# Kernel tuning notes

Hardware: AMD Instinct MI355X
Metric: run time of the kernel (lower is better)

The kernel has to match this reference:

```python
import jax, jax.numpy as jnp
import numpy as np

N_NODES = 50000


def gcn_conv(x, W, b, src, dst, n_nodes):
    # PyG GCNConv: y = D^-1/2 (A + I) D^-1/2 (x @ W) + b, with D counting self-loops
    h = x @ W                                             # [N, out]
    deg = jnp.ones((n_nodes,), h.dtype).at[dst].add(1.0)  # in-degree + self-loop
    dinv = jax.lax.rsqrt(deg)
    norm = dinv[src] * dinv[dst]                          # [E]
    msg = h[src] * norm[:, None]                          # [E, out]
    out = jnp.zeros_like(h).at[dst].add(msg)              # scatter-add over edges
    out = out + h * (dinv * dinv)[:, None]                # self-loop contribution
    return out + b


def setup_inputs() -> dict:
    key = jax.random.key(0)
    k = jax.random.split(key, 7)
    d_in, d_hid, d_out = 128, 128, 64
    x = jax.random.normal(k[0], (N_NODES, d_in), jnp.float32)
    edge_index = jax.random.randint(k[1], (2, 800000), 0, N_NODES, jnp.int64)
    s1 = 1.0 / np.sqrt(d_in)
    s2 = 1.0 / np.sqrt(d_hid)
    W1 = jax.random.uniform(k[2], (d_in, d_hid), jnp.float32, -s1, s1)
    b1 = jnp.zeros((d_hid,), jnp.float32)
    W2 = jax.random.uniform(k[3], (d_hid, d_out), jnp.float32, -s2, s2)
    b2 = jnp.zeros((d_out,), jnp.float32)
    return {"x": x, "edge_index": edge_index, "W1": W1, "b1": b1, "W2": W2, "b2": b2}


def reference(x, edge_index, W1, b1, W2, b2):
    src, dst = edge_index[0], edge_index[1]
    h = jax.nn.relu(gcn_conv(x, W1, b1, src, dst, N_NODES))
    h = gcn_conv(h, W2, b2, src, dst, N_NODES)
    return jax.nn.log_softmax(h, axis=1)
```

## Files before the change

### kernel.cpp

```cpp
#include <hip/hip_runtime.h>
#include <hip/hip_bf16.h>
#include <math.h>


typedef unsigned int uint32;
typedef unsigned short ushort16;
typedef unsigned char uchar;
typedef __attribute__((ext_vector_type(8))) short bf16x8;
typedef __attribute__((ext_vector_type(4))) float f32x4;

__device__ inline unsigned short f2bf_rne(float f) {
    uint32 x = __float_as_uint(f);
    uint32 r = (x + 0x7fffu + ((x >> 16) & 1u)) >> 16;
    return (unsigned short)r;
}
__device__ inline uint32 pack_bf16x2(float a, float b) {
    return (uint32)f2bf_rne(a) | ((uint32)f2bf_rne(b) << 16);
}
__device__ inline float2 unpack_bf16x2(uint32 u) {
    float2 r;
    r.x = __uint_as_float(u << 16);
    r.y = __uint_as_float(u & 0xffff0000u);
    return r;
}

#define NHB 128

__global__ __launch_bounds__(256) void hist_conv_k(const int* __restrict__ dst, int E,
                                                   int NWb, int chunk,
                                                   uint32* __restrict__ counts_pb,
                                                   uchar* __restrict__ rankx,
                                                   const float* __restrict__ W1,
                                                   const float* __restrict__ W2,
                                                   unsigned short* __restrict__ W1t,
                                                   unsigned short* __restrict__ W2t) {
    const int tid = threadIdx.x;
    if ((int)blockIdx.x >= 4 * NHB) {
        int idx = ((int)blockIdx.x - 4 * NHB) * 256 + tid;
        if (idx < 128 * 128) {
            int ns = idx >> 7, k = idx & 127;
            int t = ns >> 4, m = ns & 15;
            int col = 32 * (t >> 1) + 2 * m + (t & 1);
            W1t[idx] = f2bf_rne(W1[k * 128 + col]);
        } else {
            int i2 = idx - 128 * 128;
            if (i2 < 64 * 128) {
                int ns = i2 >> 7, k = i2 & 127;
                int t = ns >> 4, m = ns & 15;
                int col = 32 * (t >> 1) + 2 * m + (t & 1);
                W2t[i2] = f2bf_rne(W2[k * 64 + col]);
            }
        }
        return;
    }
    extern __shared__ uint32 sh[];
    const int hb  = blockIdx.x >> 2;
    const int qt  = blockIdx.x & 3;
    const int NWq = (NWb + 3) >> 2;
    const int qlo = qt * NWq;
    const int qhi = min(NWb, qlo + NWq);
    const int qn  = qhi - qlo;
    for (int i = tid; i < qn; i += 256) sh[i] = 0;
    __syncthreads();
    const int e0 = hb * chunk;
    const int e1 = min(E, e0 + chunk);
    int e = e0 + tid;
    for (; e + 768 < e1; e += 1024) {
        int d0 = dst[e];
        int d1 = dst[e + 256];
        int d2 = dst[e + 512];
        int d3 = dst[e + 768];
        int w0 = d0 >> 2, w1 = d1 >> 2, w2 = d2 >> 2, w3 = d3 >> 2;
        if (w0 >= qlo && w0 < qhi) {
            uint32 o = atomicAdd(&sh[w0 - qlo], 1u << (8 * (d0 & 3)));
            rankx[e] = (uchar)(o >> (8 * (d0 & 3)));
        }
        if (w1 >= qlo && w1 < qhi) {
            uint32 o = atomicAdd(&sh[w1 - qlo], 1u << (8 * (d1 & 3)));
            rankx[e + 256] = (uchar)(o >> (8 * (d1 & 3)));
        }
        if (w2 >= qlo && w2 < qhi) {
            uint32 o = atomicAdd(&sh[w2 - qlo], 1u << (8 * (d2 & 3)));
            rankx[e + 512] = (uchar)(o >> (8 * (d2 & 3)));
        }
        if (w3 >= qlo && w3 < qhi) {
            uint32 o = atomicAdd(&sh[w3 - qlo], 1u << (8 * (d3 & 3)));
            rankx[e + 768] = (uchar)(o >> (8 * (d3 & 3)));
        }
    }
    for (; e < e1; e += 256) {
        int d = dst[e];
        int w = d >> 2;
        if (w >= qlo && w < qhi) {
            uint32 o = atomicAdd(&sh[w - qlo], 1u << (8 * (d & 3)));
            rankx[e] = (uchar)(o >> (8 * (d & 3)));
        }
    }
    __syncthreads();
    uint32* dstp = counts_pb + (size_t)hb * NWb + qlo;
    for (int i = tid; i < qn; i += 256) dstp[i] = sh[i];
}

__global__ __launch_bounds__(256) void scan2_k(const uint32* __restrict__ counts_pb,
                                               int N, int NWb,
                                               uchar* __restrict__ basecum,
                                               int* __restrict__ exscan,
                                               int* __restrict__ blocksum,
                                               float* __restrict__ dinv,
                                               ushort16* __restrict__ degs) {
    __shared__ int sd[256];
    const int tid = threadIdx.x;
    const int n   = blockIdx.x * 256 + tid;
    const int nc  = n < N ? n : N - 1;
    const int wq  = nc >> 2;
    const int sh8 = 8 * (nc & 3);
    int cum = 0;
    for (int bb = 0; bb < NHB; bb += 16) {
        uint32 wv[16];
#pragma unroll
        for (int j = 0; j < 16; ++j)
            wv[j] = counts_pb[(size_t)(bb + j) * NWb + wq];
#pragma unroll
        for (int j = 0; j < 16; ++j) {
            int c = (int)((wv[j] >> sh8) & 0xffu);
            if (n < N) basecum[(size_t)(bb + j) * N + n] = (uchar)cum;
            cum += c;
        }
    }
    int v = (n < N) ? cum : 0;
    if (n < N) {
        dinv[n] = rsqrtf((float)(v + 1));
        degs[n] = (ushort16)v;
    }
    int vp = (v + 7) & ~7;
    sd[tid] = vp;
    __syncthreads();
    for (int off = 1; off < 256; off <<= 1) {
        int t = (tid >= off) ? sd[tid - off] : 0;
        __syncthreads();
        sd[tid] += t;
        __syncthreads();
    }
    if (n < N) exscan[n] = sd[tid] - vp;
    if (tid == 255) blocksum[blockIdx.x] = sd[255];
}

__global__ __launch_bounds__(256) void fill_gemm1_k(const int* __restrict__ src,
                                                    const int* __restrict__ dst, int E,
                                                    int chunk, int N,
                                                    const uchar* __restrict__ rankx,
                                                    const uchar* __restrict__ basecum,
                                                    const int* __restrict__ blocksum,
                                                    int NB,
                                                    const int* __restrict__ exscan,
                                                    const ushort16* __restrict__ degs,
                                                    int* __restrict__ offsets,
                                                    ushort16* __restrict__ csr_src,
                                                    const float* __restrict__ X,
                                                    const unsigned short* __restrict__ Wt,
                                                    const float* __restrict__ dinv,
                                                    uint32* __restrict__ Yu, int Nrows) {
    __shared__ int sd[256];
    __shared__ int ebs[256];
    __shared__ int total;
    if ((int)blockIdx.x < 256) {
        const int f   = blockIdx.x;
        const int tid = threadIdx.x;
        int v = (tid < NB) ? blocksum[tid] : 0;
        sd[tid] = v;
        __syncthreads();
        for (int off = 1; off < 256; off <<= 1) {
            int t = (tid >= off) ? sd[tid - off] : 0;
            __syncthreads();
            sd[tid] += t;
            __syncthreads();
        }
        ebs[tid] = sd[tid] - v;
        if (tid == 255) total = sd[255];
        __syncthreads();
        int g = f * 256 + tid;
        if (g < N) {
            int off = ebs[g >> 8] + exscan[g];
            offsets[g] = off;
            int dg = degs[g];
            int pl = (dg + 7) & ~7;
            for (int k = dg; k < pl; ++k) csr_src[off + k] = (ushort16)N;
        } else if (g == N) {
            offsets[N] = total;
        }
        const int b  = f >> 1;
        const uchar* bc = basecum + (size_t)b * N;
        const int q2 = chunk >> 1;
        const int e0 = b * chunk + (f & 1) * q2;
        const int e1 = min(E, e0 + q2);
        int e = e0 + tid;
        for (; e + 768 < e1; e += 1024) {
#pragma unroll
            for (int j = 0; j < 4; ++j) {
                int ej = e + j * 256;
                int d = dst[ej];
                int pos = ebs[d >> 8] + exscan[d] + (int)bc[d] + (int)rankx[ej];
                csr_src[pos] = (ushort16)src[ej];
            }
        }
        for (; e < e1; e += 256) {
            int d = dst[e];
            int pos = ebs[d >> 8] + exscan[d] + (int)bc[d] + (int)rankx[e];
            csr_src[pos] = (ushort16)src[e];
        }
        return;
    }
    constexpr int NCOL = 128;
    constexpr int NT = NCOL / 16;
    const int tid  = threadIdx.x;
    const int wave = tid >> 6;
    const int lane = tid & 63;
    const int m16  = lane & 15;
    const int q    = lane >> 4;
    const int r0   = ((int)blockIdx.x - 256) * 64 + wave * 16;

    if ((int)blockIdx.x == 256 && tid < 64) Yu[(size_t)Nrows * (NCOL / 2) + tid] = 0;

    int arow = r0 + m16;
    if (arow >= Nrows) arow = Nrows - 1;

    bf16x8 afrag[4];
#pragma unroll
    for (int kb = 0; kb < 4; ++kb) {
        const float* p = &X[(size_t)arow * 128 + kb * 32 + q * 8];
        float4 u0 = *(const float4*)p;
        float4 u1 = *(const float4*)(p + 4);
        bf16x8 a;
        a[0] = (short)f2bf_rne(u0.x); a[1] = (short)f2bf_rne(u0.y);
        a[2] = (short)f2bf_rne(u0.z); a[3] = (short)f2bf_rne(u0.w);
        a[4] = (short)f2bf_rne(u1.x); a[5] = (short)f2bf_rne(u1.y);
        a[6] = (short)f2bf_rne(u1.z); a[7] = (short)f2bf_rne(u1.w);
        afrag[kb] = a;
    }

    f32x4 acc[NT];
#pragma unroll
    for (int t = 0; t < NT; ++t) acc[t] = (f32x4){0.f, 0.f, 0.f, 0.f};
#pragma unroll
    for (int t = 0; t < NT; ++t) {
        const unsigned short* Bp = &Wt[(size_t)(t * 16 + m16) * 128 + q * 8];
#pragma unroll
        for (int kb = 0; kb < 4; ++kb) {
            bf16x8 bfrag = *(const bf16x8*)&Bp[kb * 32];
            acc[t] = __builtin_amdgcn_mfma_f32_16x16x32_bf16(afrag[kb], bfrag, acc[t], 0, 0, 0);
        }
    }
#pragma unroll
    for (int i = 0; i < 4; ++i) {
        int row = r0 + q * 4 + i;
        if (row < Nrows) {
            float dn = dinv[row];
#pragma unroll
            for (int u = 0; u < NT / 2; ++u)
                Yu[(size_t)row * (NCOL / 2) + u * 16 + m16] =
                    pack_bf16x2(acc[2 * u][i] * dn, acc[2 * u + 1][i] * dn);
        }
    }
}

__global__ __launch_bounds__(256, 8) void agg1_gemm2_k(const unsigned short* __restrict__ hs,
                                                       const int* __restrict__ offsets,
                                                       const ushort16* __restrict__ csr_src,
                                                       const float* __restrict__ dinv,
                                                       const float* __restrict__ b1,
                                                       const unsigned short* __restrict__ W2t,
                                                       uint32* __restrict__ Yu, int N) {
    __shared__ uint32 srow[16 * 68];
    const int tid  = threadIdx.x;
    const int w    = tid >> 6;
    const int lane = tid & 63;
    const int base = (int)blockIdx.x * 16;
    const uint32* T = (const uint32*)hs;
    const float2 bb = ((const float2*)b1)[lane];
    if (blockIdx.x == 0 && w == 2 && lane < 32) Yu[(size_t)N * 32 + lane] = 0;
#pragma unroll
    for (int which = 0; which < 4; ++which) {
        const int node = base + 4 * w + which;
        uint32 packed = 0;
        if (node < N) {
            const int start = offsets[node];
            const int end   = offsets[node + 1];
            const float dn  = dinv[node];
            float2 self = unpack_bf16x2(T[(size_t)node * 64 + lane]);
            float ax0 = self.x, ay0 = self.y;
            float ax1 = 0.f, ay1 = 0.f, ax2 = 0.f, ay2 = 0.f, ax3 = 0.f, ay3 = 0.f;
            int p = start;
            for (; p + 15 < end; p += 16) {
                uint4 ia = *(const uint4*)&csr_src[p];
                uint4 ib = *(const uint4*)&csr_src[p + 8];
                int s0 = ia.x & 0xffff, s1 = ia.x >> 16;
                int s2 = ia.y & 0xffff, s3 = ia.y >> 16;
                int s4 = ia.z & 0xffff, s5 = ia.z >> 16;
                int s6 = ia.w & 0xffff, s7 = ia.w >> 16;
                int s8 = ib.x & 0xffff, s9 = ib.x >> 16;
                int sa = ib.y & 0xffff, sb = ib.y >> 16;
                int sc = ib.z & 0xffff, sd = ib.z >> 16;
                int se = ib.w & 0xffff, sf = ib.w >> 16;
                uint32 u0 = T[(size_t)s0 * 64 + lane];
                uint32 u1 = T[(size_t)s1 * 64 + lane];
                uint32 u2 = T[(size_t)s2 * 64 + lane];
                uint32 u3 = T[(size_t)s3 * 64 + lane];
                uint32 u4 = T[(size_t)s4 * 64 + lane];
                uint32 u5 = T[(size_t)s5 * 64 + lane];
                uint32 u6 = T[(size_t)s6 * 64 + lane];
                uint32 u7 = T[(size_t)s7 * 64 + lane];
                uint32 u8 = T[(size_t)s8 * 64 + lane];
                uint32 u9 = T[(size_t)s9 * 64 + lane];
                uint32 ua = T[(size_t)sa * 64 + lane];
                uint32 ub = T[(size_t)sb * 64 + lane];
                uint32 uc = T[(size_t)sc * 64 + lane];
                uint32 ud = T[(size_t)sd * 64 + lane];
                uint32 ue = T[(size_t)se * 64 + lane];
                uint32 uf = T[(size_t)sf * 64 + lane];
                float2 f0 = unpack_bf16x2(u0), f1 = unpack_bf16x2(u1);
                float2 f2 = unpack_bf16x2(u2), f3 = unpack_bf16x2(u3);
                float2 f4 = unpack_bf16x2(u4), f5 = unpack_bf16x2(u5);
                float2 f6 = unpack_bf16x2(u6), f7 = unpack_bf16x2(u7);
                float2 f8 = unpack_bf16x2(u8), f9 = unpack_bf16x2(u9);
                float2 fa = unpack_bf16x2(ua), fb = unpack_bf16x2(ub);
                float2 fc = unpack_bf16x2(uc), fd = unpack_bf16x2(ud);
                float2 fe = unpack_bf16x2(ue), ff = unpack_bf16x2(uf);
                ax0 += (f0.x + f4.x) + (f8.x + fc.x);
                ay0 += (f0.y + f4.y) + (f8.y + fc.y);
                ax1 += (f1.x + f5.x) + (f9.x + fd.x);
                ay1 += (f1.y + f5.y) + (f9.y + fd.y);
                ax2 += (f2.x + f6.x) + (fa.x + fe.x);
                ay2 += (f2.y + f6.y) + (fa.y + fe.y);
                ax3 += (f3.x + f7.x) + (fb.x + ff.x);
                ay3 += (f3.y + f7.y) + (fb.y + ff.y);
            }
            for (; p + 7 < end; p += 8) {
                uint4 ia = *(const uint4*)&csr_src[p];
                int s0 = ia.x & 0xffff, s1 = ia.x >> 16;
                int s2 = ia.y & 0xffff, s3 = ia.y >> 16;
                int s4 = ia.z & 0xffff, s5 = ia.z >> 16;
                int s6 = ia.w & 0xffff, s7 = ia.w >> 16;
                uint32 u0 = T[(size_t)s0 * 64 + lane];
                uint32 u1 = T[(size_t)s1 * 64 + lane];
                uint32 u2 = T[(size_t)s2 * 64 + lane];
                uint32 u3 = T[(size_t)s3 * 64 + lane];
                uint32 u4 = T[(size_t)s4 * 64 + lane];
                uint32 u5 = T[(size_t)s5 * 64 + lane];
                uint32 u6 = T[(size_t)s6 * 64 + lane];
                uint32 u7 = T[(size_t)s7 * 64 + lane];
                float2 f0 = unpack_bf16x2(u0), f1 = unpack_bf16x2(u1);
                float2 f2 = unpack_bf16x2(u2), f3 = unpack_bf16x2(u3);
                float2 f4 = unpack_bf16x2(u4), f5 = unpack_bf16x2(u5);
                float2 f6 = unpack_bf16x2(u6), f7 = unpack_bf16x2(u7);
                ax0 += f0.x + f4.x; ay0 += f0.y + f4.y;
                ax1 += f1.x + f5.x; ay1 += f1.y + f5.y;
                ax2 += f2.x + f6.x; ay2 += f2.y + f6.y;
                ax3 += f3.x + f7.x; ay3 += f3.y + f7.y;
            }
            float vx = ((ax0 + ax1) + (ax2 + ax3)) * dn + bb.x;
            float vy = ((ay0 + ay1) + (ay2 + ay3)) * dn + bb.y;
            vx = vx > 0.f ? vx : 0.f;
            vy = vy > 0.f ? vy : 0.f;
            packed = pack_bf16x2(vx, vy);
        }
        srow[(4 * w + which) * 68 + lane] = packed;
    }
    __syncthreads();
    if (w < 2) {
        const int pp  = w;
        const int m16 = lane & 15;
        const int q   = lane >> 4;
        bf16x8 afrag[4];
#pragma unroll
        for (int kb = 0; kb < 4; ++kb)
            afrag[kb] = *(const bf16x8*)&srow[m16 * 68 + kb * 16 + q * 4];
        f32x4 acc0 = (f32x4){0.f, 0.f, 0.f, 0.f};
        f32x4 acc1 = (f32x4){0.f, 0.f, 0.f, 0.f};
        const unsigned short* Bp0 = &W2t[(size_t)((2 * pp) * 16 + m16) * 128 + q * 8];
        const unsigned short* Bp1 = &W2t[(size_t)((2 * pp + 1) * 16 + m16) * 128 + q * 8];
#pragma unroll
        for (int kb = 0; kb < 4; ++kb) {
            bf16x8 b0  = *(const bf16x8*)&Bp0[kb * 32];
            bf16x8 b1f = *(const bf16x8*)&Bp1[kb * 32];
            acc0 = __builtin_amdgcn_mfma_f32_16x16x32_bf16(afrag[kb], b0, acc0, 0, 0, 0);
            acc1 = __builtin_amdgcn_mfma_f32_16x16x32_bf16(afrag[kb], b1f, acc1, 0, 0, 0);
        }
#pragma unroll
        for (int i = 0; i < 4; ++i) {
            int row = base + q * 4 + i;
            if (row < N) {
                float dn2 = dinv[row];
                Yu[(size_t)row * 32 + pp * 16 + m16] =
                    pack_bf16x2(acc0[i] * dn2, acc1[i] * dn2);
            }
        }
    }
}

__global__ __launch_bounds__(256, 8) void agg2_k(const unsigned short* __restrict__ hs,
                                                 const int* __restrict__ offsets,
                                                 const ushort16* __restrict__ csr_src,
                                                 const float* __restrict__ dinv,
                                                 const float* __restrict__ b2,
                                                 float* __restrict__ out, int N) {
    const int tid  = threadIdx.x;
    const int node = blockIdx.x * 8 + (tid >> 5);
    const int l    = tid & 31;
    if (node >= N) return;
    const uint32* T = (const uint32*)hs;
    const int start = offsets[node];
    const int end   = offsets[node + 1];
    const float dn  = dinv[node];
    float2 self = unpack_bf16x2(T[(size_t)node * 32 + l]);
    float ax0 = self.x, ay0 = self.y;
    float ax1 = 0.f, ay1 = 0.f, ax2 = 0.f, ay2 = 0.f, ax3 = 0.f, ay3 = 0.f;
    int p = start;
    for (; p + 15 < end; p += 16) {
        uint4 ia = *(const uint4*)&csr_src[p];
        uint4 ib = *(const uint4*)&csr_src[p + 8];
        int s0 = ia.x & 0xffff, s1 = ia.x >> 16;
        int s2 = ia.y & 0xffff, s3 = ia.y >> 16;
        int s4 = ia.z & 0xffff, s5 = ia.z >> 16;
        int s6 = ia.w & 0xffff, s7 = ia.w >> 16;
        int s8 = ib.x & 0xffff, s9 = ib.x >> 16;
        int sa = ib.y & 0xffff, sb = ib.y >> 16;
        int sc = ib.z & 0xffff, sd = ib.z >> 16;
        int se = ib.w & 0xffff, sf = ib.w >> 16;
        uint32 u0 = T[(size_t)s0 * 32 + l];
        uint32 u1 = T[(size_t)s1 * 32 + l];
        uint32 u2 = T[(size_t)s2 * 32 + l];
        uint32 u3 = T[(size_t)s3 * 32 + l];
        uint32 u4 = T[(size_t)s4 * 32 + l];
        uint32 u5 = T[(size_t)s5 * 32 + l];
        uint32 u6 = T[(size_t)s6 * 32 + l];
        uint32 u7 = T[(size_t)s7 * 32 + l];
        uint32 u8 = T[(size_t)s8 * 32 + l];
        uint32 u9 = T[(size_t)s9 * 32 + l];
        uint32 ua = T[(size_t)sa * 32 + l];
        uint32 ub = T[(size_t)sb * 32 + l];
        uint32 uc = T[(size_t)sc * 32 + l];
        uint32 ud = T[(size_t)sd * 32 + l];
        uint32 ue = T[(size_t)se * 32 + l];
        uint32 uf = T[(size_t)sf * 32 + l];
        float2 f0 = unpack_bf16x2(u0), f1 = unpack_bf16x2(u1);
        float2 f2 = unpack_bf16x2(u2), f3 = unpack_bf16x2(u3);
        float2 f4 = unpack_bf16x2(u4), f5 = unpack_bf16x2(u5);
        float2 f6 = unpack_bf16x2(u6), f7 = unpack_bf16x2(u7);
        float2 f8 = unpack_bf16x2(u8), f9 = unpack_bf16x2(u9);
        float2 fa = unpack_bf16x2(ua), fb = unpack_bf16x2(ub);
        float2 fc = unpack_bf16x2(uc), fd = unpack_bf16x2(ud);
        float2 fe = unpack_bf16x2(ue), ff = unpack_bf16x2(uf);
        ax0 += (f0.x + f4.x) + (f8.x + fc.x);
        ay0 += (f0.y + f4.y) + (f8.y + fc.y);
        ax1 += (f1.x + f5.x) + (f9.x + fd.x);
        ay1 += (f1.y + f5.y) + (f9.y + fd.y);
        ax2 += (f2.x + f6.x) + (fa.x + fe.x);
        ay2 += (f2.y + f6.y) + (fa.y + fe.y);
        ax3 += (f3.x + f7.x) + (fb.x + ff.x);
        ay3 += (f3.y + f7.y) + (fb.y + ff.y);
    }
    for (; p + 7 < end; p += 8) {
        uint4 ia = *(const uint4*)&csr_src[p];
        int s0 = ia.x & 0xffff, s1 = ia.x >> 16;
        int s2 = ia.y & 0xffff, s3 = ia.y >> 16;
        int s4 = ia.z & 0xffff, s5 = ia.z >> 16;
        int s6 = ia.w & 0xffff, s7 = ia.w >> 16;
        uint32 u0 = T[(size_t)s0 * 32 + l];
        uint32 u1 = T[(size_t)s1 * 32 + l];
        uint32 u2 = T[(size_t)s2 * 32 + l];
        uint32 u3 = T[(size_t)s3 * 32 + l];
        uint32 u4 = T[(size_t)s4 * 32 + l];
        uint32 u5 = T[(size_t)s5 * 32 + l];
        uint32 u6 = T[(size_t)s6 * 32 + l];
        uint32 u7 = T[(size_t)s7 * 32 + l];
        float2 f0 = unpack_bf16x2(u0), f1 = unpack_bf16x2(u1);
        float2 f2 = unpack_bf16x2(u2), f3 = unpack_bf16x2(u3);
        float2 f4 = unpack_bf16x2(u4), f5 = unpack_bf16x2(u5);
        float2 f6 = unpack_bf16x2(u6), f7 = unpack_bf16x2(u7);
        ax0 += f0.x + f4.x; ay0 += f0.y + f4.y;
        ax1 += f1.x + f5.x; ay1 += f1.y + f5.y;
        ax2 += f2.x + f6.x; ay2 += f2.y + f6.y;
        ax3 += f3.x + f7.x; ay3 += f3.y + f7.y;
    }
    float2 bb = ((const float2*)b2)[l];
    float vx = ((ax0 + ax1) + (ax2 + ax3)) * dn + bb.x;
    float vy = ((ay0 + ay1) + (ay2 + ay3)) * dn + bb.y;
    float m = fmaxf(vx, vy);
#pragma unroll
    for (int off = 16; off > 0; off >>= 1) m = fmaxf(m, __shfl_xor(m, off, 64));
    float ex = __expf(vx - m) + __expf(vy - m);
    float ssum = ex;
#pragma unroll
    for (int off = 16; off > 0; off >>= 1) ssum += __shfl_xor(ssum, off, 64);
    float lse = m + __logf(ssum);
    float2 o = {vx - lse, vy - lse};
    ((float2*)out)[(size_t)node * 32 + l] = o;
}

extern "C" void kernel_launch(void* const* d_in, const int* in_sizes, int n_in,
                              void* d_out, int out_size, void* d_ws, size_t ws_size,
                              hipStream_t stream) {
    const float* x  = (const float*)d_in[0];
    const int*   ei = (const int*)d_in[1];
    const float* W1 = (const float*)d_in[2];
    const float* b1 = (const float*)d_in[3];
    const float* W2 = (const float*)d_in[4];
    const float* b2 = (const float*)d_in[5];
    float* out = (float*)d_out;

    const int N = in_sizes[0] / 128;
    const int E = in_sizes[1] / 2;
    const int* src = ei;
    const int* dst = ei + E;
    const int NB = (N + 255) / 256;
    const int NWb = (N + 3) / 4;
    const int NWq = (NWb + 3) >> 2;
    const int chunk = (E + NHB - 1) / NHB;

    char* ws = (char*)d_ws;
    auto alloc = [&](size_t bytes) -> char* {
        char* p = ws;
        ws += (bytes + 255) & ~(size_t)255;
        return p;
    };
    unsigned short* h1  = (unsigned short*)alloc((size_t)(N + 1) * 128 * 2);
    unsigned short* h2  = (unsigned short*)alloc((size_t)(N + 1) * 64 * 2);
    uint32* counts_pb = (uint32*)alloc((size_t)NHB * NWb * 4);
    uchar* basecum  = (uchar*)alloc((size_t)NHB * N);
    uchar* rankx    = (uchar*)alloc((size_t)E);
    ushort16* csr_src = (ushort16*)alloc(((size_t)E + 8 * (size_t)N) * 2);
    float* dinv     = (float*)alloc((size_t)N * 4);
    int*   exscan   = (int*)alloc((size_t)N * 4);
    int*   blocksum = (int*)alloc((size_t)NB * 4);
    int*   offsets  = (int*)alloc((size_t)(N + 1) * 4);
    ushort16* degs  = (ushort16*)alloc((size_t)N * 2);
    unsigned short* W1t = (unsigned short*)alloc(128 * 128 * 2);
    unsigned short* W2t = (unsigned short*)alloc(64 * 128 * 2);

    const int GB = (N + 63) / 64;
    const int CB = (128 * 128 + 64 * 128 + 255) / 256;

    hist_conv_k<<<4 * NHB + CB, 256, NWq * 4, stream>>>(dst, E, NWb, chunk, counts_pb,
                                                        rankx, W1, W2, W1t, W2t);
    scan2_k<<<NB, 256, 0, stream>>>(counts_pb, N, NWb, basecum, exscan, blocksum, dinv,
                                    degs);
    fill_gemm1_k<<<256 + GB, 256, 0, stream>>>(src, dst, E, chunk, N, rankx, basecum,
                                               blocksum, NB, exscan, degs, offsets,
                                               csr_src, x, W1t, dinv, (uint32*)h1, N);
    agg1_gemm2_k<<<(N + 15) / 16, 256, 0, stream>>>(h1, offsets, csr_src, dinv, b1,
                                                    W2t, (uint32*)h2, N);
    agg2_k<<<(N + 7) / 8, 256, 0, stream>>>(h2, offsets, csr_src, dinv, b2, out, N);
}
```

Baseline: 174.8 us.

## Merge five kernels into two cooperative persistent kernels with grid syncs

```diff
diff --git a/kernel.cpp b/kernel.cpp
--- a/kernel.cpp
+++ b/kernel.cpp
@@ -1,6 +1,9 @@
 #include <hip/hip_runtime.h>
 #include <hip/hip_bf16.h>
+#include <hip/hip_cooperative_groups.h>
 #include <math.h>
+
+namespace cg = cooperative_groups;
 
 
 typedef unsigned int uint32;
@@ -25,149 +28,111 @@
 }
 
 #define NHB 128
-
-__global__ __launch_bounds__(256) void hist_conv_k(const int* __restrict__ dst, int E,
-                                                   int NWb, int chunk,
-                                                   uint32* __restrict__ counts_pb,
-                                                   uchar* __restrict__ rankx,
-                                                   const float* __restrict__ W1,
-                                                   const float* __restrict__ W2,
-                                                   unsigned short* __restrict__ W1t,
-                                                   unsigned short* __restrict__ W2t) {
+#define HCB 96
+
+__global__ __launch_bounds__(256) void mega1_k(
+    const int* __restrict__ dst, int E, int NWb, int chunk,
+    uint32* __restrict__ counts_pb, uchar* __restrict__ rankx,
+    const float* __restrict__ W1, const float* __restrict__ W2,
+    unsigned short* __restrict__ W1t, unsigned short* __restrict__ W2t,
+    int N, uchar* __restrict__ basecum, int* __restrict__ exscan,
+    int* __restrict__ blocksum, float* __restrict__ dinv,
+    ushort16* __restrict__ degs, int NB, int NU) {
+    extern __shared__ uint32 sh[];
+    __shared__ int sd[256];
     const int tid = threadIdx.x;
-    if ((int)blockIdx.x >= 4 * NHB) {
-        int idx = ((int)blockIdx.x - 4 * NHB) * 256 + tid;
-        if (idx < 128 * 128) {
-            int ns = idx >> 7, k = idx & 127;
-            int t = ns >> 4, m = ns & 15;
-            int col = 32 * (t >> 1) + 2 * m + (t & 1);
-            W1t[idx] = f2bf_rne(W1[k * 128 + col]);
-        } else {
-            int i2 = idx - 128 * 128;
-            if (i2 < 64 * 128) {
-                int ns = i2 >> 7, k = i2 & 127;
+    for (int u = blockIdx.x; u < NU; u += gridDim.x) {
+        if (u >= 4 * NHB) {
+            int idx = (u - 4 * NHB) * 256 + tid;
+            if (idx < 128 * 128) {
+                int ns = idx >> 7, k = idx & 127;
                 int t = ns >> 4, m = ns & 15;
                 int col = 32 * (t >> 1) + 2 * m + (t & 1);
-                W2t[i2] = f2bf_rne(W2[k * 64 + col]);
-            }
-        }
-        return;
+                W1t[idx] = f2bf_rne(W1[k * 128 + col]);
+            } else {
+                int i2 = idx - 128 * 128;
+                if (i2 < 64 * 128) {
+                    int ns = i2 >> 7, k = i2 & 127;
+                    int t = ns >> 4, m = ns & 15;
+                    int col = 32 * (t >> 1) + 2 * m + (t & 1);
+                    W2t[i2] = f2bf_rne(W2[k * 64 + col]);
+                }
+            }
+        } else {
+            const int hb  = u >> 2;
+            const int qt  = u & 3;
+            const int NWq = (NWb + 3) >> 2;
+            const int qlo = qt * NWq;
+            const int qhi = min(NWb, qlo + NWq);
+            const int qn  = qhi - qlo;
+            for (int i = tid; i < qn; i += 256) sh[i] = 0;
+            __syncthreads();
+            const int e0 = hb * chunk;
+            const int e1 = min(E, e0 + chunk);
+            int e = e0 + tid;
+            for (; e + 768 < e1; e += 1024) {
+                int d0 = dst[e];
+                int d1 = dst[e + 256];
+                int d2 = dst[e + 512];
+                int d3 = dst[e + 768];
+                int w0 = d0 >> 2, w1 = d1 >> 2, w2 = d2 >> 2, w3 = d3 >> 2;
+                if (w0 >= qlo && w0 < qhi) {
+                    uint32 o = atomicAdd(&sh[w0 - qlo], 1u << (8 * (d0 & 3)));
+                    rankx[e] = (uchar)(o >> (8 * (d0 & 3)));
+                }
+                if (w1 >= qlo && w1 < qhi) {
+                    uint32 o = atomicAdd(&sh[w1 - qlo], 1u << (8 * (d1 & 3)));
+                    rankx[e + 256] = (uchar)(o >> (8 * (d1 & 3)));
+                }
+                if (w2 >= qlo && w2 < qhi) {
+                    uint32 o = atomicAdd(&sh[w2 - qlo], 1u << (8 * (d2 & 3)));
+                    rankx[e + 512] = (uchar)(o >> (8 * (d2 & 3)));
+                }
+                if (w3 >= qlo && w3 < qhi) {
+                    uint32 o = atomicAdd(&sh[w3 - qlo], 1u << (8 * (d3 & 3)));
+                    rankx[e + 768] = (uchar)(o >> (8 * (d3 & 3)));
+                }
+            }
+            for (; e < e1; e += 256) {
+                int d = dst[e];
+                int w = d >> 2;
+                if (w >= qlo && w < qhi) {
+                    uint32 o = atomicAdd(&sh[w - qlo], 1u << (8 * (d & 3)));
+                    rankx[e] = (uchar)(o >> (8 * (d & 3)));
+                }
+            }
+            __syncthreads();
+            uint32* dstp = counts_pb + (size_t)hb * NWb + qlo;
+            for (int i = tid; i < qn; i += 256) dstp[i] = sh[i];
+            __syncthreads();
+        }
     }
-    extern __shared__ uint32 sh[];
-    const int hb  = blockIdx.x >> 2;
-    const int qt  = blockIdx.x & 3;
-    const int NWq = (NWb + 3) >> 2;
-    const int qlo = qt * NWq;
-    const int qhi = min(NWb, qlo + NWq);
-    const int qn  = qhi - qlo;
-    for (int i = tid; i < qn; i += 256) sh[i] = 0;
-    __syncthreads();
-    const int e0 = hb * chunk;
-    const int e1 = min(E, e0 + chunk);
-    int e = e0 + tid;
-    for (; e + 768 < e1; e += 1024) {
-        int d0 = dst[e];
-        int d1 = dst[e + 256];
-        int d2 = dst[e + 512];
-        int d3 = dst[e + 768];
-        int w0 = d0 >> 2, w1 = d1 >> 2, w2 = d2 >> 2, w3 = d3 >> 2;
-        if (w0 >= qlo && w0 < qhi) {
-            uint32 o = atomicAdd(&sh[w0 - qlo], 1u << (8 * (d0 & 3)));
-            rankx[e] = (uchar)(o >> (8 * (d0 & 3)));
-        }
-        if (w1 >= qlo && w1 < qhi) {
-            uint32 o = atomicAdd(&sh[w1 - qlo], 1u << (8 * (d1 & 3)));
-            rankx[e + 256] = (uchar)(o >> (8 * (d1 & 3)));
-        }
-        if (w2 >= qlo && w2 < qhi) {
-            uint32 o = atomicAdd(&sh[w2 - qlo], 1u << (8 * (d2 & 3)));
-            rankx[e + 512] = (uchar)(o >> (8 * (d2 & 3)));
-        }
-        if (w3 >= qlo && w3 < qhi) {
-            uint32 o = atomicAdd(&sh[w3 - qlo], 1u << (8 * (d3 & 3)));
-            rankx[e + 768] = (uchar)(o >> (8 * (d3 & 3)));
-        }
-    }
-    for (; e < e1; e += 256) {
-        int d = dst[e];
-        int w = d >> 2;
-        if (w >= qlo && w < qhi) {
-            uint32 o = atomicAdd(&sh[w - qlo], 1u << (8 * (d & 3)));
-            rankx[e] = (uchar)(o >> (8 * (d & 3)));
-        }
-    }
-    __syncthreads();
-    uint32* dstp = counts_pb + (size_t)hb * NWb + qlo;
-    for (int i = tid; i < qn; i += 256) dstp[i] = sh[i];
-}
-
-__global__ __launch_bounds__(256) void scan2_k(const uint32* __restrict__ counts_pb,
-                                               int N, int NWb,
-                                               uchar* __restrict__ basecum,
-                                               int* __restrict__ exscan,
-                                               int* __restrict__ blocksum,
-                                               float* __restrict__ dinv,
-                                               ushort16* __restrict__ degs) {
-    __shared__ int sd[256];
-    const int tid = threadIdx.x;
-    const int n   = blockIdx.x * 256 + tid;
-    const int nc  = n < N ? n : N - 1;
-    const int wq  = nc >> 2;
-    const int sh8 = 8 * (nc & 3);
-    int cum = 0;
-    for (int bb = 0; bb < NHB; bb += 16) {
-        uint32 wv[16];
-#pragma unroll
-        for (int j = 0; j < 16; ++j)
-            wv[j] = counts_pb[(size_t)(bb + j) * NWb + wq];
-#pragma unroll
-        for (int j = 0; j < 16; ++j) {
-            int c = (int)((wv[j] >> sh8) & 0xffu);
-            if (n < N) basecum[(size_t)(bb + j) * N + n] = (uchar)cum;
-            cum += c;
-        }
-    }
-    int v = (n < N) ? cum : 0;
-    if (n < N) {
-        dinv[n] = rsqrtf((float)(v + 1));
-        degs[n] = (ushort16)v;
-    }
-    int vp = (v + 7) & ~7;
-    sd[tid] = vp;
-    __syncthreads();
-    for (int off = 1; off < 256; off <<= 1) {
-        int t = (tid >= off) ? sd[tid - off] : 0;
-        __syncthreads();
-        sd[tid] += t;
-        __syncthreads();
-    }
-    if (n < N) exscan[n] = sd[tid] - vp;
-    if (tid == 255) blocksum[blockIdx.x] = sd[255];
-}
-
-__global__ __launch_bounds__(256) void fill_gemm1_k(const int* __restrict__ src,
-                                                    const int* __restrict__ dst, int E,
-                                                    int chunk, int N,
-                                                    const uchar* __restrict__ rankx,
-                                                    const uchar* __restrict__ basecum,
-                                                    const int* __restrict__ blocksum,
-                                                    int NB,
-                                                    const int* __restrict__ exscan,
-                                                    const ushort16* __restrict__ degs,
-                                                    int* __restrict__ offsets,
-                                                    ushort16* __restrict__ csr_src,
-                                                    const float* __restrict__ X,
-                                                    const unsigned short* __restrict__ Wt,
-                                                    const float* __restrict__ dinv,
-                                                    uint32* __restrict__ Yu, int Nrows) {
-    __shared__ int sd[256];
-    __shared__ int ebs[256];
-    __shared__ int total;
-    if ((int)blockIdx.x < 256) {
-        const int f   = blockIdx.x;
-        const int tid = threadIdx.x;
-        int v = (tid < NB) ? blocksum[tid] : 0;
-        sd[tid] = v;
+    cg::this_grid().sync();
+    for (int u = blockIdx.x; u < NB; u += gridDim.x) {
+        const int n  = u * 256 + tid;
+        const int nc = n < N ? n : N - 1;
+        const int wq  = nc >> 2;
+        const int sh8 = 8 * (nc & 3);
+        int cum = 0;
+        for (int bb = 0; bb < NHB; bb += 16) {
+            uint32 wv[16];
+#pragma unroll
+            for (int j = 0; j < 16; ++j)
+                wv[j] = counts_pb[(size_t)(bb + j) * NWb + wq];
+#pragma unroll
+            for (int j = 0; j < 16; ++j) {
+                int c = (int)((wv[j] >> sh8) & 0xffu);
+                if (n < N) basecum[(size_t)(bb + j) * N + n] = (uchar)cum;
+                cum += c;
+            }
+        }
+        int v = (n < N) ? cum : 0;
+        if (n < N) {
+            dinv[n] = rsqrtf((float)(v + 1));
+            degs[n] = (ushort16)v;
+        }
+        int vp = (v + 7) & ~7;
+        sd[tid] = vp;
         __syncthreads();
         for (int off = 1; off < 256; off <<= 1) {
             int t = (tid >= off) ? sd[tid - off] : 0;
@@ -175,326 +140,340 @@
             sd[tid] += t;
             __syncthreads();
         }
-        ebs[tid] = sd[tid] - v;
-        if (tid == 255) total = sd[255];
+        if (n < N) exscan[n] = sd[tid] - vp;
+        if (tid == 255) blocksum[u] = sd[255];
         __syncthreads();
-        int g = f * 256 + tid;
-        if (g < N) {
-            int off = ebs[g >> 8] + exscan[g];
-            offsets[g] = off;
-            int dg = degs[g];
-            int pl = (dg + 7) & ~7;
-            for (int k = dg; k < pl; ++k) csr_src[off + k] = (ushort16)N;
-        } else if (g == N) {
-            offsets[N] = total;
-        }
-        const int b  = f >> 1;
-        const uchar* bc = basecum + (size_t)b * N;
-        const int q2 = chunk >> 1;
-        const int e0 = b * chunk + (f & 1) * q2;
-        const int e1 = min(E, e0 + q2);
-        int e = e0 + tid;
-        for (; e + 768 < e1; e += 1024) {
-#pragma unroll
-            for (int j = 0; j < 4; ++j) {
-                int ej = e + j * 256;
-                int d = dst[ej];
-                int pos = ebs[d >> 8] + exscan[d] + (int)bc[d] + (int)rankx[ej];
-                csr_src[pos] = (ushort16)src[ej];
-            }
-        }
-        for (; e < e1; e += 256) {
-            int d = dst[e];
-            int pos = ebs[d >> 8] + exscan[d] + (int)bc[d] + (int)rankx[e];
-            csr_src[pos] = (ushort16)src[e];
-        }
-        return;
-    }
-    constexpr int NCOL = 128;
-    constexpr int NT = NCOL / 16;
-    const int tid  = threadIdx.x;
-    const int wave = tid >> 6;
-    const int lane = tid & 63;
-    const int m16  = lane & 15;
-    const int q    = lane >> 4;
-    const int r0   = ((int)blockIdx.x - 256) * 64 + wave * 16;
-
-    if ((int)blockIdx.x == 256 && tid < 64) Yu[(size_t)Nrows * (NCOL / 2) + tid] = 0;
-
-    int arow = r0 + m16;
-    if (arow >= Nrows) arow = Nrows - 1;
-
-    bf16x8 afrag[4];
-#pragma unroll
-    for (int kb = 0; kb < 4; ++kb) {
-        const float* p = &X[(size_t)arow * 128 + kb * 32 + q * 8];
-        float4 u0 = *(const float4*)p;
-        float4 u1 = *(const float4*)(p + 4);
-        bf16x8 a;
-        a[0] = (short)f2bf_rne(u0.x); a[1] = (short)f2bf_rne(u0.y);
-        a[2] = (short)f2bf_rne(u0.z); a[3] = (short)f2bf_rne(u0.w);
-        a[4] = (short)f2bf_rne(u1.x); a[5] = (short)f2bf_rne(u1.y);
-        a[6] = (short)f2bf_rne(u1.z); a[7] = (short)f2bf_rne(u1.w);
-        afrag[kb] = a;
-    }
-
-    f32x4 acc[NT];
-#pragma unroll
-    for (int t = 0; t < NT; ++t) acc[t] = (f32x4){0.f, 0.f, 0.f, 0.f};
-#pragma unroll
-    for (int t = 0; t < NT; ++t) {
-        const unsigned short* Bp = &Wt[(size_t)(t * 16 + m16) * 128 + q * 8];
-#pragma unroll
-        for (int kb = 0; kb < 4; ++kb) {
-            bf16x8 bfrag = *(const bf16x8*)&Bp[kb * 32];
-            acc[t] = __builtin_amdgcn_mfma_f32_16x16x32_bf16(afrag[kb], bfrag, acc[t], 0, 0, 0);
-        }
-    }
-#pragma unroll
-    for (int i = 0; i < 4; ++i) {
-        int row = r0 + q * 4 + i;
-        if (row < Nrows) {
-            float dn = dinv[row];
-#pragma unroll
-            for (int u = 0; u < NT / 2; ++u)
-                Yu[(size_t)row * (NCOL / 2) + u * 16 + m16] =
-                    pack_bf16x2(acc[2 * u][i] * dn, acc[2 * u + 1][i] * dn);
-        }
     }
 }
 
-__global__ __launch_bounds__(256, 8) void agg1_gemm2_k(const unsigned short* __restrict__ hs,
-                                                       const int* __restrict__ offsets,
-                                                       const ushort16* __restrict__ csr_src,
-                                                       const float* __restrict__ dinv,
-                                                       const float* __restrict__ b1,
-                                                       const unsigned short* __restrict__ W2t,
-                                                       uint32* __restrict__ Yu, int N) {
+__global__ __launch_bounds__(256) void mega2_k(
+    const int* __restrict__ src, const int* __restrict__ dst, int E, int chunk,
+    int N, const uchar* __restrict__ rankx, const uchar* __restrict__ basecum,
+    const int* __restrict__ blocksum, int NB, const int* __restrict__ exscan,
+    const ushort16* __restrict__ degs, int* __restrict__ offsets,
+    ushort16* __restrict__ csr_src, const float* __restrict__ X,
+    const unsigned short* __restrict__ W1t, const float* __restrict__ dinv,
+    uint32* __restrict__ Y1, const unsigned short* __restrict__ W2t,
+    uint32* __restrict__ Y2, const float* __restrict__ b1,
+    const float* __restrict__ b2, float* __restrict__ out, int GB) {
+    __shared__ int sd[256];
+    __shared__ int ebs[256];
     __shared__ uint32 srow[16 * 68];
     const int tid  = threadIdx.x;
     const int w    = tid >> 6;
     const int lane = tid & 63;
-    const int base = (int)blockIdx.x * 16;
-    const uint32* T = (const uint32*)hs;
-    const float2 bb = ((const float2*)b1)[lane];
-    if (blockIdx.x == 0 && w == 2 && lane < 32) Yu[(size_t)N * 32 + lane] = 0;
-#pragma unroll
-    for (int which = 0; which < 4; ++which) {
-        const int node = base + 4 * w + which;
-        uint32 packed = 0;
-        if (node < N) {
-            const int start = offsets[node];
-            const int end   = offsets[node + 1];
-            const float dn  = dinv[node];
-            float2 self = unpack_bf16x2(T[(size_t)node * 64 + lane]);
-            float ax0 = self.x, ay0 = self.y;
-            float ax1 = 0.f, ay1 = 0.f, ax2 = 0.f, ay2 = 0.f, ax3 = 0.f, ay3 = 0.f;
-            int p = start;
-            for (; p + 15 < end; p += 16) {
-                uint4 ia = *(const uint4*)&csr_src[p];
-                uint4 ib = *(const uint4*)&csr_src[p + 8];
-                int s0 = ia.x & 0xffff, s1 = ia.x >> 16;
-                int s2 = ia.y & 0xffff, s3 = ia.y >> 16;
-                int s4 = ia.z & 0xffff, s5 = ia.z >> 16;
-                int s6 = ia.w & 0xffff, s7 = ia.w >> 16;
-                int s8 = ib.x & 0xffff, s9 = ib.x >> 16;
-                int sa = ib.y & 0xffff, sb = ib.y >> 16;
-                int sc = ib.z & 0xffff, sd = ib.z >> 16;
-                int se = ib.w & 0xffff, sf = ib.w >> 16;
-                uint32 u0 = T[(size_t)s0 * 64 + lane];
-                uint32 u1 = T[(size_t)s1 * 64 + lane];
-                uint32 u2 = T[(size_t)s2 * 64 + lane];
-                uint32 u3 = T[(size_t)s3 * 64 + lane];
-                uint32 u4 = T[(size_t)s4 * 64 + lane];
-                uint32 u5 = T[(size_t)s5 * 64 + lane];
-                uint32 u6 = T[(size_t)s6 * 64 + lane];
-                uint32 u7 = T[(size_t)s7 * 64 + lane];
-                uint32 u8 = T[(size_t)s8 * 64 + lane];
-                uint32 u9 = T[(size_t)s9 * 64 + lane];
-                uint32 ua = T[(size_t)sa * 64 + lane];
-                uint32 ub = T[(size_t)sb * 64 + lane];
-                uint32 uc = T[(size_t)sc * 64 + lane];
-                uint32 ud = T[(size_t)sd * 64 + lane];
-                uint32 ue = T[(size_t)se * 64 + lane];
-                uint32 uf = T[(size_t)sf * 64 + lane];
-                float2 f0 = unpack_bf16x2(u0), f1 = unpack_bf16x2(u1);
-                float2 f2 = unpack_bf16x2(u2), f3 = unpack_bf16x2(u3);
-                float2 f4 = unpack_bf16x2(u4), f5 = unpack_bf16x2(u5);
-                float2 f6 = unpack_bf16x2(u6), f7 = unpack_bf16x2(u7);
-                float2 f8 = unpack_bf16x2(u8), f9 = unpack_bf16x2(u9);
-                float2 fa = unpack_bf16x2(ua), fb = unpack_bf16x2(ub);
-                float2 fc = unpack_bf16x2(uc), fd = unpack_bf16x2(ud);
-                float2 fe = unpack_bf16x2(ue), ff = unpack_bf16x2(uf);
-                ax0 += (f0.x + f4.x) + (f8.x + fc.x);
-                ay0 += (f0.y + f4.y) + (f8.y + fc.y);
-                ax1 += (f1.x + f5.x) + (f9.x + fd.x);
-                ay1 += (f1.y + f5.y) + (f9.y + fd.y);
-                ax2 += (f2.x + f6.x) + (fa.x + fe.x);
-                ay2 += (f2.y + f6.y) + (fa.y + fe.y);
-                ax3 += (f3.x + f7.x) + (fb.x + ff.x);
-                ay3 += (f3.y + f7.y) + (fb.y + ff.y);
-            }
-            for (; p + 7 < end; p += 8) {
-                uint4 ia = *(const uint4*)&csr_src[p];
-                int s0 = ia.x & 0xffff, s1 = ia.x >> 16;
-                int s2 = ia.y & 0xffff, s3 = ia.y >> 16;
-                int s4 = ia.z & 0xffff, s5 = ia.z >> 16;
-                int s6 = ia.w & 0xffff, s7 = ia.w >> 16;
-                uint32 u0 = T[(size_t)s0 * 64 + lane];
-                uint32 u1 = T[(size_t)s1 * 64 + lane];
-                uint32 u2 = T[(size_t)s2 * 64 + lane];
-                uint32 u3 = T[(size_t)s3 * 64 + lane];
-                uint32 u4 = T[(size_t)s4 * 64 + lane];
-                uint32 u5 = T[(size_t)s5 * 64 + lane];
-                uint32 u6 = T[(size_t)s6 * 64 + lane];
-                uint32 u7 = T[(size_t)s7 * 64 + lane];
-                float2 f0 = unpack_bf16x2(u0), f1 = unpack_bf16x2(u1);
-                float2 f2 = unpack_bf16x2(u2), f3 = unpack_bf16x2(u3);
-                float2 f4 = unpack_bf16x2(u4), f5 = unpack_bf16x2(u5);
-                float2 f6 = unpack_bf16x2(u6), f7 = unpack_bf16x2(u7);
-                ax0 += f0.x + f4.x; ay0 += f0.y + f4.y;
-                ax1 += f1.x + f5.x; ay1 += f1.y + f5.y;
-                ax2 += f2.x + f6.x; ay2 += f2.y + f6.y;
-                ax3 += f3.x + f7.x; ay3 += f3.y + f7.y;
-            }
-            float vx = ((ax0 + ax1) + (ax2 + ax3)) * dn + bb.x;
-            float vy = ((ay0 + ay1) + (ay2 + ay3)) * dn + bb.y;
-            vx = vx > 0.f ? vx : 0.f;
-            vy = vy > 0.f ? vy : 0.f;
-            packed = pack_bf16x2(vx, vy);
-        }
-        srow[(4 * w + which) * 68 + lane] = packed;
+    const int NU1 = 256 + GB;
+    for (int u = blockIdx.x; u < NU1; u += gridDim.x) {
+        if (u < 256) {
+            int v = (tid < NB) ? blocksum[tid] : 0;
+            sd[tid] = v;
+            __syncthreads();
+            for (int off = 1; off < 256; off <<= 1) {
+                int t = (tid >= off) ? sd[tid - off] : 0;
+                __syncthreads();
+                sd[tid] += t;
+                __syncthreads();
+            }
+            ebs[tid] = sd[tid] - v;
+            __syncthreads();
+            int total = sd[255];
+            int g = u * 256 + tid;
+            if (g < N) {
+                int off = ebs[g >> 8] + exscan[g];
+                offsets[g] = off;
+                int dg = degs[g];
+                int pl = (dg + 7) & ~7;
+                for (int k = dg; k < pl; ++k) csr_src[off + k] = (ushort16)N;
+            } else if (g == N) {
+                offsets[N] = total;
+            }
+            const int b  = u >> 1;
+            const uchar* bc = basecum + (size_t)b * N;
+            const int q2 = chunk >> 1;
+            const int e0 = b * chunk + (u & 1) * q2;
+            const int e1 = min(E, e0 + q2);
+            int e = e0 + tid;
+            for (; e + 768 < e1; e += 1024) {
+#pragma unroll
+                for (int j = 0; j < 4; ++j) {
+                    int ej = e + j * 256;
+                    int d = dst[ej];
+                    int pos = ebs[d >> 8] + exscan[d] + (int)bc[d] + (int)rankx[ej];
+                    csr_src[pos] = (ushort16)src[ej];
+                }
+            }
+            for (; e < e1; e += 256) {
+                int d = dst[e];
+                int pos = ebs[d >> 8] + exscan[d] + (int)bc[d] + (int)rankx[e];
+                csr_src[pos] = (ushort16)src[e];
+            }
+            __syncthreads();
+        } else {
+            const int m16 = lane & 15;
+            const int q   = lane >> 4;
+            const int r0  = (u - 256) * 64 + w * 16;
+            if (u == 256 && tid < 64) Y1[(size_t)N * 64 + tid] = 0;
+            int arow = r0 + m16;
+            if (arow >= N) arow = N - 1;
+            bf16x8 afrag[4];
+#pragma unroll
+            for (int kb = 0; kb < 4; ++kb) {
+                const float* p = &X[(size_t)arow * 128 + kb * 32 + q * 8];
+                float4 u0 = *(const float4*)p;
+                float4 u1 = *(const float4*)(p + 4);
+                bf16x8 a;
+                a[0] = (short)f2bf_rne(u0.x); a[1] = (short)f2bf_rne(u0.y);
+                a[2] = (short)f2bf_rne(u0.z); a[3] = (short)f2bf_rne(u0.w);
+                a[4] = (short)f2bf_rne(u1.x); a[5] = (short)f2bf_rne(u1.y);
+                a[6] = (short)f2bf_rne(u1.z); a[7] = (short)f2bf_rne(u1.w);
+                afrag[kb] = a;
+            }
+#pragma unroll
+            for (int pu = 0; pu < 4; ++pu) {
+                f32x4 acc0 = (f32x4){0.f, 0.f, 0.f, 0.f};
+                f32x4 acc1 = (f32x4){0.f, 0.f, 0.f, 0.f};
+                const unsigned short* Bp0 = &W1t[(size_t)((2 * pu) * 16 + m16) * 128 + q * 8];
+                const unsigned short* Bp1 = &W1t[(size_t)((2 * pu + 1) * 16 + m16) * 128 + q * 8];
+#pragma unroll
+                for (int kb = 0; kb < 4; ++kb) {
+                    bf16x8 b0  = *(const bf16x8*)&Bp0[kb * 32];
+                    bf16x8 b1f = *(const bf16x8*)&Bp1[kb * 32];
+                    acc0 = __builtin_amdgcn_mfma_f32_16x16x32_bf16(afrag[kb], b0, acc0, 0, 0, 0);
+                    acc1 = __builtin_amdgcn_mfma_f32_16x16x32_bf16(afrag[kb], b1f, acc1, 0, 0, 0);
+                }
+#pragma unroll
+                for (int i = 0; i < 4; ++i) {
+                    int row = r0 + q * 4 + i;
+                    if (row < N) {
+                        float dn = dinv[row];
+                        Y1[(size_t)row * 64 + pu * 16 + m16] =
+                            pack_bf16x2(acc0[i] * dn, acc1[i] * dn);
+                    }
+                }
+            }
+        }
     }
-    __syncthreads();
-    if (w < 2) {
-        const int pp  = w;
-        const int m16 = lane & 15;
-        const int q   = lane >> 4;
-        bf16x8 afrag[4];
-#pragma unroll
-        for (int kb = 0; kb < 4; ++kb)
-            afrag[kb] = *(const bf16x8*)&srow[m16 * 68 + kb * 16 + q * 4];
-        f32x4 acc0 = (f32x4){0.f, 0.f, 0.f, 0.f};
-        f32x4 acc1 = (f32x4){0.f, 0.f, 0.f, 0.f};
-        const unsigned short* Bp0 = &W2t[(size_t)((2 * pp) * 16 + m16) * 128 + q * 8];
-        const unsigned short* Bp1 = &W2t[(size_t)((2 * pp + 1) * 16 + m16) * 128 + q * 8];
-#pragma unroll
-        for (int kb = 0; kb < 4; ++kb) {
-            bf16x8 b0  = *(const bf16x8*)&Bp0[kb * 32];
-            bf16x8 b1f = *(const bf16x8*)&Bp1[kb * 32];
-            acc0 = __builtin_amdgcn_mfma_f32_16x16x32_bf16(afrag[kb], b0, acc0, 0, 0, 0);
-            acc1 = __builtin_amdgcn_mfma_f32_16x16x32_bf16(afrag[kb], b1f, acc1, 0, 0, 0);
-        }
-#pragma unroll
-        for (int i = 0; i < 4; ++i) {
-            int row = base + q * 4 + i;
-            if (row < N) {
-                float dn2 = dinv[row];
-                Yu[(size_t)row * 32 + pp * 16 + m16] =
-                    pack_bf16x2(acc0[i] * dn2, acc1[i] * dn2);
-            }
-        }
+    cg::this_grid().sync();
+    const uint32* T = Y1;
+    const float2 bb1 = ((const float2*)b1)[lane];
+    if (blockIdx.x == 0 && tid < 32) Y2[(size_t)N * 32 + tid] = 0;
+    const int NT2 = (N + 15) / 16;
+    for (int t2 = (int)blockIdx.x; t2 < NT2; t2 += gridDim.x) {
+        const int base = t2 * 16;
+#pragma unroll
+        for (int which = 0; which < 4; ++which) {
+            const int node = base + 4 * w + which;
+            uint32 packed = 0;
+            if (node < N) {
+                const int start = offsets[node];
+                const int end   = offsets[node + 1];
+                const float dn  = dinv[node];
+                float2 self = unpack_bf16x2(T[(size_t)node * 64 + lane]);
+                float ax0 = self.x, ay0 = self.y;
+                float ax1 = 0.f, ay1 = 0.f, ax2 = 0.f, ay2 = 0.f, ax3 = 0.f, ay3 = 0.f;
+                int p = start;
+                for (; p + 15 < end; p += 16) {
+                    uint4 ia = *(const uint4*)&csr_src[p];
+                    uint4 ib = *(const uint4*)&csr_src[p + 8];
+                    int s0 = ia.x & 0xffff, s1 = ia.x >> 16;
+                    int s2 = ia.y & 0xffff, s3 = ia.y >> 16;
+                    int s4 = ia.z & 0xffff, s5 = ia.z >> 16;
+                    int s6 = ia.w & 0xffff, s7 = ia.w >> 16;
+                    int s8 = ib.x & 0xffff, s9 = ib.x >> 16;
+                    int sa = ib.y & 0xffff, sb = ib.y >> 16;
+                    int sc = ib.z & 0xffff, sdx = ib.z >> 16;
+                    int se = ib.w & 0xffff, sf = ib.w >> 16;
+                    uint32 u0 = T[(size_t)s0 * 64 + lane];
+                    uint32 u1 = T[(size_t)s1 * 64 + lane];
+                    uint32 u2 = T[(size_t)s2 * 64 + lane];
+                    uint32 u3 = T[(size_t)s3 * 64 + lane];
+                    uint32 u4 = T[(size_t)s4 * 64 + lane];
+                    uint32 u5 = T[(size_t)s5 * 64 + lane];
+                    uint32 u6 = T[(size_t)s6 * 64 + lane];
+                    uint32 u7 = T[(size_t)s7 * 64 + lane];
+                    uint32 u8 = T[(size_t)s8 * 64 + lane];
+                    uint32 u9 = T[(size_t)s9 * 64 + lane];
+                    uint32 ua = T[(size_t)sa * 64 + lane];
+                    uint32 ub = T[(size_t)sb * 64 + lane];
+                    uint32 uc = T[(size_t)sc * 64 + lane];
+                    uint32 ud = T[(size_t)sdx * 64 + lane];
+                    uint32 ue = T[(size_t)se * 64 + lane];
+                    uint32 uf = T[(size_t)sf * 64 + lane];
+                    float2 f0 = unpack_bf16x2(u0), f1 = unpack_bf16x2(u1);
+                    float2 f2 = unpack_bf16x2(u2), f3 = unpack_bf16x2(u3);
+                    float2 f4 = unpack_bf16x2(u4), f5 = unpack_bf16x2(u5);
+                    float2 f6 = unpack_bf16x2(u6), f7 = unpack_bf16x2(u7);
+                    float2 f8 = unpack_bf16x2(u8), f9 = unpack_bf16x2(u9);
+                    float2 fa = unpack_bf16x2(ua), fb = unpack_bf16x2(ub);
+                    float2 fc = unpack_bf16x2(uc), fd = unpack_bf16x2(ud);
+                    float2 fe = unpack_bf16x2(ue), ff = unpack_bf16x2(uf);
+                    ax0 += (f0.x + f4.x) + (f8.x + fc.x);
+                    ay0 += (f0.y + f4.y) + (f8.y + fc.y);
+                    ax1 += (f1.x + f5.x) + (f9.x + fd.x);
+                    ay1 += (f1.y + f5.y) + (f9.y + fd.y);
+                    ax2 += (f2.x + f6.x) + (fa.x + fe.x);
+                    ay2 += (f2.y + f6.y) + (fa.y + fe.y);
+                    ax3 += (f3.x + f7.x) + (fb.x + ff.x);
+                    ay3 += (f3.y + f7.y) + (fb.y + ff.y);
+                }
+                for (; p + 7 < end; p += 8) {
+                    uint4 ia = *(const uint4*)&csr_src[p];
+                    int s0 = ia.x & 0xffff, s1 = ia.x >> 16;
+                    int s2 = ia.y & 0xffff, s3 = ia.y >> 16;
+                    int s4 = ia.z & 0xffff, s5 = ia.z >> 16;
+                    int s6 = ia.w & 0xffff, s7 = ia.w >> 16;
+                    uint32 u0 = T[(size_t)s0 * 64 + lane];
+                    uint32 u1 = T[(size_t)s1 * 64 + lane];
+                    uint32 u2 = T[(size_t)s2 * 64 + lane];
+                    uint32 u3 = T[(size_t)s3 * 64 + lane];
+                    uint32 u4 = T[(size_t)s4 * 64 + lane];
+                    uint32 u5 = T[(size_t)s5 * 64 + lane];
+                    uint32 u6 = T[(size_t)s6 * 64 + lane];
+                    uint32 u7 = T[(size_t)s7 * 64 + lane];
+                    float2 f0 = unpack_bf16x2(u0), f1 = unpack_bf16x2(u1);
+                    float2 f2 = unpack_bf16x2(u2), f3 = unpack_bf16x2(u3);
+                    float2 f4 = unpack_bf16x2(u4), f5 = unpack_bf16x2(u5);
+                    float2 f6 = unpack_bf16x2(u6), f7 = unpack_bf16x2(u7);
+                    ax0 += f0.x + f4.x; ay0 += f0.y + f4.y;
+                    ax1 += f1.x + f5.x; ay1 += f1.y + f5.y;
+                    ax2 += f2.x + f6.x; ay2 += f2.y + f6.y;
+                    ax3 += f3.x + f7.x; ay3 += f3.y + f7.y;
+                }
+                float vx = ((ax0 + ax1) + (ax2 + ax3)) * dn + bb1.x;
+                float vy = ((ay0 + ay1) + (ay2 + ay3)) * dn + bb1.y;
+                vx = vx > 0.f ? vx : 0.f;
+                vy = vy > 0.f ? vy : 0.f;
+                packed = pack_bf16x2(vx, vy);
+            }
+            srow[(4 * w + which) * 68 + lane] = packed;
+        }
+        __syncthreads();
+        if (w < 2) {
+            const int pp  = w;
+            const int m16 = lane & 15;
+            const int q   = lane >> 4;
+            bf16x8 afrag[4];
+#pragma unroll
+            for (int kb = 0; kb < 4; ++kb)
+                afrag[kb] = *(const bf16x8*)&srow[m16 * 68 + kb * 16 + q * 4];
+            f32x4 acc0 = (f32x4){0.f, 0.f, 0.f, 0.f};
+            f32x4 acc1 = (f32x4){0.f, 0.f, 0.f, 0.f};
+            const unsigned short* Bp0 = &W2t[(size_t)((2 * pp) * 16 + m16) * 128 + q * 8];
+            const unsigned short* Bp1 = &W2t[(size_t)((2 * pp + 1) * 16 + m16) * 128 + q * 8];
+#pragma unroll
+            for (int kb = 0; kb < 4; ++kb) {
+                bf16x8 b0  = *(const bf16x8*)&Bp0[kb * 32];
+                bf16x8 b1f = *(const bf16x8*)&Bp1[kb * 32];
+                acc0 = __builtin_amdgcn_mfma_f32_16x16x32_bf16(afrag[kb], b0, acc0, 0, 0, 0);
+                acc1 = __builtin_amdgcn_mfma_f32_16x16x32_bf16(afrag[kb], b1f, acc1, 0, 0, 0);
+            }
+#pragma unroll
+            for (int i = 0; i < 4; ++i) {
+                int row = base + q * 4 + i;
+                if (row < N) {
+                    float dn2 = dinv[row];
+                    Y2[(size_t)row * 32 + pp * 16 + m16] =
+                        pack_bf16x2(acc0[i] * dn2, acc1[i] * dn2);
+                }
+            }
+        }
+        __syncthreads();
     }
-}
-
-__global__ __launch_bounds__(256, 8) void agg2_k(const unsigned short* __restrict__ hs,
-                                                 const int* __restrict__ offsets,
-                                                 const ushort16* __restrict__ csr_src,
-                                                 const float* __restrict__ dinv,
-                                                 const float* __restrict__ b2,
-                                                 float* __restrict__ out, int N) {
-    const int tid  = threadIdx.x;
-    const int node = blockIdx.x * 8 + (tid >> 5);
-    const int l    = tid & 31;
-    if (node >= N) return;
-    const uint32* T = (const uint32*)hs;
-    const int start = offsets[node];
-    const int end   = offsets[node + 1];
-    const float dn  = dinv[node];
-    float2 self = unpack_bf16x2(T[(size_t)node * 32 + l]);
-    float ax0 = self.x, ay0 = self.y;
-    float ax1 = 0.f, ay1 = 0.f, ax2 = 0.f, ay2 = 0.f, ax3 = 0.f, ay3 = 0.f;
-    int p = start;
-    for (; p + 15 < end; p += 16) {
-        uint4 ia = *(const uint4*)&csr_src[p];
-        uint4 ib = *(const uint4*)&csr_src[p + 8];
-        int s0 = ia.x & 0xffff, s1 = ia.x >> 16;
-        int s2 = ia.y & 0xffff, s3 = ia.y >> 16;
-        int s4 = ia.z & 0xffff, s5 = ia.z >> 16;
-        int s6 = ia.w & 0xffff, s7 = ia.w >> 16;
-        int s8 = ib.x & 0xffff, s9 = ib.x >> 16;
-        int sa = ib.y & 0xffff, sb = ib.y >> 16;
-        int sc = ib.z & 0xffff, sd = ib.z >> 16;
-        int se = ib.w & 0xffff, sf = ib.w >> 16;
-        uint32 u0 = T[(size_t)s0 * 32 + l];
-        uint32 u1 = T[(size_t)s1 * 32 + l];
-        uint32 u2 = T[(size_t)s2 * 32 + l];
-        uint32 u3 = T[(size_t)s3 * 32 + l];
-        uint32 u4 = T[(size_t)s4 * 32 + l];
-        uint32 u5 = T[(size_t)s5 * 32 + l];
-        uint32 u6 = T[(size_t)s6 * 32 + l];
-        uint32 u7 = T[(size_t)s7 * 32 + l];
-        uint32 u8 = T[(size_t)s8 * 32 + l];
-        uint32 u9 = T[(size_t)s9 * 32 + l];
-        uint32 ua = T[(size_t)sa * 32 + l];
-        uint32 ub = T[(size_t)sb * 32 + l];
-        uint32 uc = T[(size_t)sc * 32 + l];
-        uint32 ud = T[(size_t)sd * 32 + l];
-        uint32 ue = T[(size_t)se * 32 + l];
-        uint32 uf = T[(size_t)sf * 32 + l];
-        float2 f0 = unpack_bf16x2(u0), f1 = unpack_bf16x2(u1);
-        float2 f2 = unpack_bf16x2(u2), f3 = unpack_bf16x2(u3);
-        float2 f4 = unpack_bf16x2(u4), f5 = unpack_bf16x2(u5);
-        float2 f6 = unpack_bf16x2(u6), f7 = unpack_bf16x2(u7);
-        float2 f8 = unpack_bf16x2(u8), f9 = unpack_bf16x2(u9);
-        float2 fa = unpack_bf16x2(ua), fb = unpack_bf16x2(ub);
-        float2 fc = unpack_bf16x2(uc), fd = unpack_bf16x2(ud);
-        float2 fe = unpack_bf16x2(ue), ff = unpack_bf16x2(uf);
-        ax0 += (f0.x + f4.x) + (f8.x + fc.x);
-        ay0 += (f0.y + f4.y) + (f8.y + fc.y);
-        ax1 += (f1.x + f5.x) + (f9.x + fd.x);
-        ay1 += (f1.y + f5.y) + (f9.y + fd.y);
-        ax2 += (f2.x + f6.x) + (fa.x + fe.x);
-        ay2 += (f2.y + f6.y) + (fa.y + fe.y);
-        ax3 += (f3.x + f7.x) + (fb.x + ff.x);
-        ay3 += (f3.y + f7.y) + (fb.y + ff.y);
+    cg::this_grid().sync();
+    const uint32* T2 = Y2;
+    const int l = tid & 31;
+    const float2 bb2 = ((const float2*)b2)[l];
+    const int NT3 = (N + 7) / 8;
+    for (int t3 = (int)blockIdx.x; t3 < NT3; t3 += gridDim.x) {
+        const int node = t3 * 8 + (tid >> 5);
+        if (node >= N) continue;
+        const int start = offsets[node];
+        const int end   = offsets[node + 1];
+        const float dn  = dinv[node];
+        float2 self = unpack_bf16x2(T2[(size_t)node * 32 + l]);
+        float ax0 = self.x, ay0 = self.y;
+        float ax1 = 0.f, ay1 = 0.f, ax2 = 0.f, ay2 = 0.f, ax3 = 0.f, ay3 = 0.f;
+        int p = start;
+        for (; p + 15 < end; p += 16) {
+            uint4 ia = *(const uint4*)&csr_src[p];
+            uint4 ib = *(const uint4*)&csr_src[p + 8];
+            int s0 = ia.x & 0xffff, s1 = ia.x >> 16;
+            int s2 = ia.y & 0xffff, s3 = ia.y >> 16;
+            int s4 = ia.z & 0xffff, s5 = ia.z >> 16;
+            int s6 = ia.w & 0xffff, s7 = ia.w >> 16;
+            int s8 = ib.x & 0xffff, s9 = ib.x >> 16;
+            int sa = ib.y & 0xffff, sb = ib.y >> 16;
+            int sc = ib.z & 0xffff, sdx = ib.z >> 16;
+            int se = ib.w & 0xffff, sf = ib.w >> 16;
+            uint32 u0 = T2[(size_t)s0 * 32 + l];
+            uint32 u1 = T2[(size_t)s1 * 32 + l];
+            uint32 u2 = T2[(size_t)s2 * 32 + l];
+            uint32 u3 = T2[(size_t)s3 * 32 + l];
+            uint32 u4 = T2[(size_t)s4 * 32 + l];
+            uint32 u5 = T2[(size_t)s5 * 32 + l];
+            uint32 u6 = T2[(size_t)s6 * 32 + l];
+            uint32 u7 = T2[(size_t)s7 * 32 + l];
+            uint32 u8 = T2[(size_t)s8 * 32 + l];
+            uint32 u9 = T2[(size_t)s9 * 32 + l];
+            uint32 ua = T2[(size_t)sa * 32 + l];
+            uint32 ub = T2[(size_t)sb * 32 + l];
+            uint32 uc = T2[(size_t)sc * 32 + l];
+            uint32 ud = T2[(size_t)sdx * 32 + l];
+            uint32 ue = T2[(size_t)se * 32 + l];
+            uint32 uf = T2[(size_t)sf * 32 + l];
+            float2 f0 = unpack_bf16x2(u0), f1 = unpack_bf16x2(u1);
+            float2 f2 = unpack_bf16x2(u2), f3 = unpack_bf16x2(u3);
+            float2 f4 = unpack_bf16x2(u4), f5 = unpack_bf16x2(u5);
+            float2 f6 = unpack_bf16x2(u6), f7 = unpack_bf16x2(u7);
+            float2 f8 = unpack_bf16x2(u8), f9 = unpack_bf16x2(u9);
+            float2 fa = unpack_bf16x2(ua), fb = unpack_bf16x2(ub);
+            float2 fc = unpack_bf16x2(uc), fd = unpack_bf16x2(ud);
+            float2 fe = unpack_bf16x2(ue), ff = unpack_bf16x2(uf);
+            ax0 += (f0.x + f4.x) + (f8.x + fc.x);
+            ay0 += (f0.y + f4.y) + (f8.y + fc.y);
+            ax1 += (f1.x + f5.x) + (f9.x + fd.x);
+            ay1 += (f1.y + f5.y) + (f9.y + fd.y);
+            ax2 += (f2.x + f6.x) + (fa.x + fe.x);
+            ay2 += (f2.y + f6.y) + (fa.y + fe.y);
+            ax3 += (f3.x + f7.x) + (fb.x + ff.x);
+            ay3 += (f3.y + f7.y) + (fb.y + ff.y);
+        }
+        for (; p + 7 < end; p += 8) {
+            uint4 ia = *(const uint4*)&csr_src[p];
+            int s0 = ia.x & 0xffff, s1 = ia.x >> 16;
+            int s2 = ia.y & 0xffff, s3 = ia.y >> 16;
+            int s4 = ia.z & 0xffff, s5 = ia.z >> 16;
+            int s6 = ia.w & 0xffff, s7 = ia.w >> 16;
+            uint32 u0 = T2[(size_t)s0 * 32 + l];
+            uint32 u1 = T2[(size_t)s1 * 32 + l];
+            uint32 u2 = T2[(size_t)s2 * 32 + l];
+            uint32 u3 = T2[(size_t)s3 * 32 + l];
+            uint32 u4 = T2[(size_t)s4 * 32 + l];
+            uint32 u5 = T2[(size_t)s5 * 32 + l];
+            uint32 u6 = T2[(size_t)s6 * 32 + l];
+            uint32 u7 = T2[(size_t)s7 * 32 + l];
+            float2 f0 = unpack_bf16x2(u0), f1 = unpack_bf16x2(u1);
+            float2 f2 = unpack_bf16x2(u2), f3 = unpack_bf16x2(u3);
+            float2 f4 = unpack_bf16x2(u4), f5 = unpack_bf16x2(u5);
+            float2 f6 = unpack_bf16x2(u6), f7 = unpack_bf16x2(u7);
+            ax0 += f0.x + f4.x; ay0 += f0.y + f4.y;
+            ax1 += f1.x + f5.x; ay1 += f1.y + f5.y;
+            ax2 += f2.x + f6.x; ay2 += f2.y + f6.y;
+            ax3 += f3.x + f7.x; ay3 += f3.y + f7.y;
+        }
+        float vx = ((ax0 + ax1) + (ax2 + ax3)) * dn + bb2.x;
+        float vy = ((ay0 + ay1) + (ay2 + ay3)) * dn + bb2.y;
+        float m = fmaxf(vx, vy);
+#pragma unroll
+        for (int off = 16; off > 0; off >>= 1) m = fmaxf(m, __shfl_xor(m, off, 64));
+        float ex = __expf(vx - m) + __expf(vy - m);
+        float ssum = ex;
+#pragma unroll
+        for (int off = 16; off > 0; off >>= 1) ssum += __shfl_xor(ssum, off, 64);
+        float lse = m + __logf(ssum);
+        float2 o = {vx - lse, vy - lse};
+        ((float2*)out)[(size_t)node * 32 + l] = o;
     }
-    for (; p + 7 < end; p += 8) {
-        uint4 ia = *(const uint4*)&csr_src[p];
-        int s0 = ia.x & 0xffff, s1 = ia.x >> 16;
-        int s2 = ia.y & 0xffff, s3 = ia.y >> 16;
-        int s4 = ia.z & 0xffff, s5 = ia.z >> 16;
-        int s6 = ia.w & 0xffff, s7 = ia.w >> 16;
-        uint32 u0 = T[(size_t)s0 * 32 + l];
-        uint32 u1 = T[(size_t)s1 * 32 + l];
-        uint32 u2 = T[(size_t)s2 * 32 + l];
-        uint32 u3 = T[(size_t)s3 * 32 + l];
-        uint32 u4 = T[(size_t)s4 * 32 + l];
-        uint32 u5 = T[(size_t)s5 * 32 + l];
-        uint32 u6 = T[(size_t)s6 * 32 + l];
-        uint32 u7 = T[(size_t)s7 * 32 + l];
-        float2 f0 = unpack_bf16x2(u0), f1 = unpack_bf16x2(u1);
-        float2 f2 = unpack_bf16x2(u2), f3 = unpack_bf16x2(u3);
-        float2 f4 = unpack_bf16x2(u4), f5 = unpack_bf16x2(u5);
-        float2 f6 = unpack_bf16x2(u6), f7 = unpack_bf16x2(u7);
-        ax0 += f0.x + f4.x; ay0 += f0.y + f4.y;
-        ax1 += f1.x + f5.x; ay1 += f1.y + f5.y;
-        ax2 += f2.x + f6.x; ay2 += f2.y + f6.y;
-        ax3 += f3.x + f7.x; ay3 += f3.y + f7.y;
-    }
-    float2 bb = ((const float2*)b2)[l];
-    float vx = ((ax0 + ax1) + (ax2 + ax3)) * dn + bb.x;
-    float vy = ((ay0 + ay1) + (ay2 + ay3)) * dn + bb.y;
-    float m = fmaxf(vx, vy);
-#pragma unroll
-    for (int off = 16; off > 0; off >>= 1) m = fmaxf(m, __shfl_xor(m, off, 64));
-    float ex = __expf(vx - m) + __expf(vy - m);
-    float ssum = ex;
-#pragma unroll
-    for (int off = 16; off > 0; off >>= 1) ssum += __shfl_xor(ssum, off, 64);
-    float lse = m + __logf(ssum);
-    float2 o = {vx - lse, vy - lse};
-    ((float2*)out)[(size_t)node * 32 + l] = o;
 }
 
 extern "C" void kernel_launch(void* const* d_in, const int* in_sizes, int n_in,
@@ -537,17 +516,46 @@
     unsigned short* W1t = (unsigned short*)alloc(128 * 128 * 2);
     unsigned short* W2t = (unsigned short*)alloc(64 * 128 * 2);
 
-    const int GB = (N + 63) / 64;
-    const int CB = (128 * 128 + 64 * 128 + 255) / 256;
-
-    hist_conv_k<<<4 * NHB + CB, 256, NWq * 4, stream>>>(dst, E, NWb, chunk, counts_pb,
-                                                        rankx, W1, W2, W1t, W2t);
-    scan2_k<<<NB, 256, 0, stream>>>(counts_pb, N, NWb, basecum, exscan, blocksum, dinv,
-                                    degs);
-    fill_gemm1_k<<<256 + GB, 256, 0, stream>>>(src, dst, E, chunk, N, rankx, basecum,
-                                               blocksum, NB, exscan, degs, offsets,
-                                               csr_src, x, W1t, dinv, (uint32*)h1, N);
-    agg1_gemm2_k<<<(N + 15) / 16, 256, 0, stream>>>(h1, offsets, csr_src, dinv, b1,
-                                                    W2t, (uint32*)h2, N);
-    agg2_k<<<(N + 7) / 8, 256, 0, stream>>>(h2, offsets, csr_src, dinv, b2, out, N);
+    const int GB  = (N + 63) / 64;
+    const int NU1 = 4 * NHB + HCB;
+
+    int mab1 = 0, mab2 = 0;
+    hipOccupancyMaxActiveBlocksPerMultiprocessor(&mab1, mega1_k, 256,
+                                                 (size_t)(NWq * 4));
+    hipOccupancyMaxActiveBlocksPerMultiprocessor(&mab2, mega2_k, 256, 0);
+    if (mab1 < 1) mab1 = 1;
+    if (mab2 < 1) mab2 = 1;
+    int G1 = NU1 < mab1 * 256 ? NU1 : mab1 * 256;
+    int cap2 = mab2 * 256;
+    int G2 = 1792 < cap2 ? 1792 : cap2;
+
+    const int* dst_a = dst; int E_a = E, NWb_a = NWb, chunk_a = chunk;
+    uint32* counts_a = counts_pb; uchar* rankx_a = rankx;
+    const float* W1_a = W1; const float* W2_a = W2;
+    unsigned short* W1t_a = W1t; unsigned short* W2t_a = W2t;
+    int N_a = N; uchar* basecum_a = basecum; int* exscan_a = exscan;
+    int* blocksum_a = blocksum; float* dinv_a = dinv; ushort16* degs_a = degs;
+    int NB_a = NB, NU_a = NU1;
+    void* a1[] = {&dst_a, &E_a, &NWb_a, &chunk_a, &counts_a, &rankx_a,
+                  &W1_a, &W2_a, &W1t_a, &W2t_a, &N_a, &basecum_a, &exscan_a,
+                  &blocksum_a, &dinv_a, &degs_a, &NB_a, &NU_a};
+    hipLaunchCooperativeKernel(mega1_k, dim3(G1), dim3(256), a1,
+                               (unsigned int)(NWq * 4), stream);
+
+    const int* src_a = src; const int* dst_b = dst;
+    int E_b = E, chunk_b = chunk, N_b = N;
+    const uchar* rankx_b = rankx; const uchar* basecum_b = basecum;
+    const int* blocksum_b = blocksum; int NB_b = NB;
+    const int* exscan_b = exscan; const ushort16* degs_b = degs;
+    int* offsets_a = offsets; ushort16* csr_a = csr_src;
+    const float* X_a = x; const unsigned short* W1t_b = W1t;
+    const float* dinv_b = dinv; uint32* Y1_a = (uint32*)h1;
+    const unsigned short* W2t_b = W2t; uint32* Y2_a = (uint32*)h2;
+    const float* b1_a = b1; const float* b2_a = b2; float* out_a = out;
+    int GB_a = GB;
+    void* a2[] = {&src_a, &dst_b, &E_b, &chunk_b, &N_b, &rankx_b, &basecum_b,
+                  &blocksum_b, &NB_b, &exscan_b, &degs_b, &offsets_a, &csr_a,
+                  &X_a, &W1t_b, &dinv_b, &Y1_a, &W2t_b, &Y2_a, &b1_a, &b2_a,
+                  &out_a, &GB_a};
+    hipLaunchCooperativeKernel(mega2_k, dim3(G2), dim3(256), a2, 0u, stream);
 }
```

Result: slower. 442.5 us (+153.1%).
